# Performance work log

Measured on AMD Instinct MI355X. Metric: run time of the kernel, lower is better.

## Reference

```python
import jax, jax.numpy as jnp
import numpy as np

QUERY_DIM = 1024
KEY_DIM = 512
HIDDEN_DIM = 128
BATCH = 32
SEQ_LEN = 2048


def setup_inputs() -> dict:
    key = jax.random.key(0)
    k1, k2, k3, k4, k5 = jax.random.split(key, 5)
    query = jax.random.normal(k1, (BATCH, QUERY_DIM), dtype=jnp.float32)
    keys = jax.random.normal(k2, (BATCH, SEQ_LEN, KEY_DIM), dtype=jnp.float32)
    # nn.Linear weights, stored as (out, in) like torch; scaled ~ kaiming-uniform bound
    W1 = jax.random.normal(k3, (HIDDEN_DIM, QUERY_DIM), dtype=jnp.float32) / np.sqrt(QUERY_DIM)
    W2 = jax.random.normal(k4, (HIDDEN_DIM, KEY_DIM), dtype=jnp.float32) / np.sqrt(KEY_DIM)
    V = jax.random.normal(k5, (1, HIDDEN_DIM), dtype=jnp.float32) / np.sqrt(HIDDEN_DIM)
    return {"query": query, "keys": keys, "W1": W1, "W2": W2, "V": V}


def reference(query, keys, W1, W2, V):
    # query: [b, q], keys: [b, s, k]
    q_proj = jnp.einsum("bq,hq->bh", query, W1)          # [b, h]
    k_proj = jnp.einsum("bsk,hk->bsh", keys, W2)          # [b, s, h]
    hidden = jnp.tanh(q_proj[:, None, :] + k_proj)        # [b, s, h]
    score = jnp.einsum("bsh,oh->bs", hidden, V)           # [b, s] (o == 1)
    attention_weights = jax.nn.softmax(score, axis=1)     # [b, s]
    context = jnp.einsum("bs,bsk->bk", attention_weights, keys)  # [b, k]
    return (context, attention_weights)
```

## Files before the change

### kernel.cpp

```cpp
#include <hip/hip_runtime.h>

#define BATCH 32
#define SEQ   2048
#define KD    512
#define QD    1024
#define HD    128

#define BM 128
#define BK 32
#define NT (KD / BK)

typedef float    f32x4 __attribute__((ext_vector_type(4)));
typedef _Float16 f16x8 __attribute__((ext_vector_type(8)));
typedef unsigned int u32;

__device__ __forceinline__ u32 pack2h(float a, float b) {
    _Float16 ha = (_Float16)a, hb = (_Float16)b;
    unsigned short ua = __builtin_bit_cast(unsigned short, ha);
    unsigned short ub = __builtin_bit_cast(unsigned short, hb);
    return (u32)ua | ((u32)ub << 16);
}

__device__ __forceinline__ void cvt16(const f32x4 a[4], uint4& h0, uint4& h1) {
    h0 = make_uint4(pack2h(a[0][0], a[0][1]), pack2h(a[0][2], a[0][3]),
                    pack2h(a[1][0], a[1][1]), pack2h(a[1][2], a[1][3]));
    h1 = make_uint4(pack2h(a[2][0], a[2][1]), pack2h(a[2][2], a[2][3]),
                    pack2h(a[3][0], a[3][1]), pack2h(a[3][2], a[3][3]));
}

__device__ __forceinline__ void gload_lds16(const void* g, void* l) {
    __builtin_amdgcn_global_load_lds(
        (const __attribute__((address_space(1))) unsigned int*)g,
        (__attribute__((address_space(3))) unsigned int*)l, 16, 0, 0);
}

__global__ __launch_bounds__(256) void prep_kernel(
        const float* __restrict__ query, const float* __restrict__ W1,
        const float* __restrict__ W2, float* __restrict__ qp,
        char* __restrict__ w2img) {
    int blk = blockIdx.x;
    int tid = threadIdx.x;
    if (blk < 512) {
        int b = blk >> 4, hg = blk & 15;
        int wave = tid >> 6, lane = tid & 63;
        int h = hg * 8 + wave * 2 + (lane >> 5);
        int l32 = lane & 31;
        const float* q = query + (size_t)b * QD;
        const float* w = W1 + (size_t)h * QD;
        float acc = 0.f;
        #pragma unroll
        for (int i = 0; i < 8; ++i) {
            float4 qv = *(const float4*)(q + i * 128 + l32 * 4);
            float4 wv = *(const float4*)(w + i * 128 + l32 * 4);
            acc += qv.x * wv.x + qv.y * wv.y + qv.z * wv.z + qv.w * wv.w;
        }
        #pragma unroll
        for (int off = 16; off >= 1; off >>= 1) acc += __shfl_xor(acc, off);
        if (l32 == 0) qp[b * HD + h] = acc;
    } else {
        int c = blk - 512;
        int row = tid >> 1;
        int scol = (tid & 1) * 16;
        const float* src = W2 + (size_t)row * KD + c * BK + scol;
        f32x4 a[4];
        #pragma unroll
        for (int i = 0; i < 4; ++i) a[i] = *(const f32x4*)(src + i * 4);
        uint4 h0, h1;
        cvt16(a, h0, h1);
        int sw = (row & 7) << 4;
        int b0 = c * 8192 + ((row * 64 + scol * 2) ^ sw);
        int b1 = c * 8192 + ((row * 64 + scol * 2 + 16) ^ sw);
        *(uint4*)(w2img + b0) = h0;
        *(uint4*)(w2img + b1) = h1;
    }
}

__global__ __launch_bounds__(256, 2) void score_ctx_kernel(
        const float* __restrict__ keys, const char* __restrict__ w2img,
        const float* __restrict__ qp, const float* __restrict__ V,
        float* __restrict__ score_out, float* __restrict__ part_m,
        float* __restrict__ part_l, float* __restrict__ part_c) {
    __shared__ __align__(16) char lds[34048];
    char* A = lds;
    char* B = lds + 16384;
    float* sc  = (float*)(lds + 32768);
    float* pb  = (float*)(lds + 32768 + 512);
    float* red = (float*)(lds + 32768 + 1024);

    const int blk = blockIdx.x;
    const int m0  = blk * BM;
    const int b   = blk >> 4;
    const int tid = threadIdx.x;
    const int wave = tid >> 6;
    const int lane = tid & 63;
    const int l15  = lane & 15;
    const int l4   = lane >> 4;

    const int srow = tid >> 1;
    const int scol = (tid & 1) * 16;
    const int ssw  = (srow & 7) << 4;
    const int sb0  = (srow * 64 + scol * 2) ^ ssw;
    const int sb1  = (srow * 64 + scol * 2 + 16) ^ ssw;
    const float* asrc = keys + (size_t)(m0 + srow) * KD + scol;

    float qv[8], vv[8];
    #pragma unroll
    for (int hj = 0; hj < 8; ++hj) {
        qv[hj] = qp[b * HD + hj * 16 + l15];
        vv[hj] = V[hj * 16 + l15];
    }

    const int boff0 = (l15 * 64 + l4 * 16) ^ ((l15 & 7) << 4);
    const int aoff0 = boff0 + wave * 2048;
    const int aoff1 = aoff0 + 1024;

    f32x4 acc[2][8];
    #pragma unroll
    for (int mi = 0; mi < 2; ++mi)
        #pragma unroll
        for (int hj = 0; hj < 8; ++hj)
            acc[mi][hj] = (f32x4)0.f;

    {
        const char* g = w2img + wave * 2048 + lane * 16;
        gload_lds16(g,        B + wave * 2048);
        gload_lds16(g + 1024, B + wave * 2048 + 1024);
        f32x4 a[4];
        #pragma unroll
        for (int i = 0; i < 4; ++i) a[i] = *(const f32x4*)(asrc + i * 4);
        uint4 h0, h1;
        cvt16(a, h0, h1);
        *(uint4*)(A + sb0) = h0;
        *(uint4*)(A + sb1) = h1;
    }
    __syncthreads();

    for (int t = 0; t < NT; ++t) {
        const int cb = t & 1, nb = cb ^ 1;
        f32x4 a[4];
        if (t + 1 < NT) {
            const char* g = w2img + (t + 1) * 8192 + wave * 2048 + lane * 16;
            gload_lds16(g,        B + nb * 8192 + wave * 2048);
            gload_lds16(g + 1024, B + nb * 8192 + wave * 2048 + 1024);
            const float* s = asrc + (t + 1) * BK;
            #pragma unroll
            for (int i = 0; i < 4; ++i) a[i] = *(const f32x4*)(s + i * 4);
        }

        f16x8 ah0 = *(const f16x8*)(A + cb * 8192 + aoff0);
        f16x8 ah1 = *(const f16x8*)(A + cb * 8192 + aoff1);
        #pragma unroll
        for (int hj = 0; hj < 8; ++hj) {
            f16x8 bh = *(const f16x8*)(B + cb * 8192 + boff0 + hj * 1024);
            acc[0][hj] = __builtin_amdgcn_mfma_f32_16x16x32_f16(ah0, bh, acc[0][hj], 0, 0, 0);
            acc[1][hj] = __builtin_amdgcn_mfma_f32_16x16x32_f16(ah1, bh, acc[1][hj], 0, 0, 0);
        }

        if (t + 1 < NT) {
            uint4 h0, h1;
            cvt16(a, h0, h1);
            *(uint4*)(A + nb * 8192 + sb0) = h0;
            *(uint4*)(A + nb * 8192 + sb1) = h1;
        }
        __syncthreads();
    }

    #pragma unroll
    for (int mi = 0; mi < 2; ++mi) {
        #pragma unroll
        for (int j = 0; j < 4; ++j) {
            float p = 0.f;
            #pragma unroll
            for (int hj = 0; hj < 8; ++hj) {
                float x = qv[hj] + acc[mi][hj][j];
                float e = __expf(2.f * x);
                float th = 1.f - 2.f * __builtin_amdgcn_rcpf(1.f + e);
                p += th * vv[hj];
            }
            #pragma unroll
            for (int off = 1; off < 16; off <<= 1) p += __shfl_xor(p, off);
            if (l15 == 0) {
                int r = wave * 32 + mi * 16 + l4 * 4 + j;
                score_out[m0 + r] = p;
                sc[r] = p;
            }
        }
    }
    __syncthreads();

    float s_val = sc[tid & 127];
    float mx = s_val;
    #pragma unroll
    for (int off = 32; off >= 1; off >>= 1) mx = fmaxf(mx, __shfl_xor(mx, off));
    if (lane == 0) red[wave] = mx;
    __syncthreads();
    float m = fmaxf(fmaxf(red[0], red[1]), fmaxf(red[2], red[3]));
    float p = __expf(s_val - m);
    if (tid < 128) pb[tid] = p;
    float ps = p;
    #pragma unroll
    for (int off = 32; off >= 1; off >>= 1) ps += __shfl_xor(ps, off);
    if (lane == 0) red[4 + wave] = ps;
    __syncthreads();
    if (tid == 0) {
        part_m[blk] = m;
        part_l[blk] = red[4] + red[5];
    }

    int col = tid * 2;
    float c0 = 0.f, c1 = 0.f;
    const float* kb = keys + (size_t)m0 * KD + col;
    #pragma unroll 4
    for (int s = 0; s < BM; ++s) {
        float w = pb[s];
        float2 kv = *(const float2*)(kb + (size_t)s * KD);
        c0 = fmaf(w, kv.x, c0);
        c1 = fmaf(w, kv.y, c1);
    }
    *(float2*)(part_c + (size_t)blk * KD + col) = make_float2(c0, c1);
}

__global__ __launch_bounds__(256) void finalize_kernel(
        const float* __restrict__ part_m, const float* __restrict__ part_l,
        const float* __restrict__ part_c, float* __restrict__ ctx,
        float* __restrict__ wts) {
    int b = blockIdx.x;
    int tid = threadIdx.x;
    float M = -1e30f;
    #pragma unroll
    for (int i = 0; i < 16; ++i) M = fmaxf(M, part_m[b * 16 + i]);
    float e[16];
    float L = 0.f;
    #pragma unroll
    for (int i = 0; i < 16; ++i) {
        e[i] = __expf(part_m[b * 16 + i] - M);
        L += e[i] * part_l[b * 16 + i];
    }
    float invL = 1.f / L;
    #pragma unroll
    for (int r = 0; r < 8; ++r) {
        int s = tid + r * 256;
        float scv = wts[b * SEQ + s];
        wts[b * SEQ + s] = __expf(scv - M) * invL;
    }
    #pragma unroll
    for (int g = 0; g < 2; ++g) {
        int col = tid + g * 256;
        float acc = 0.f;
        #pragma unroll
        for (int i = 0; i < 16; ++i)
            acc += e[i] * part_c[(size_t)(b * 16 + i) * KD + col];
        ctx[b * KD + col] = acc * invL;
    }
}

extern "C" void kernel_launch(void* const* d_in, const int* in_sizes, int n_in,
                              void* d_out, int out_size, void* d_ws, size_t ws_size,
                              hipStream_t stream) {
    const float* query = (const float*)d_in[0];
    const float* keys  = (const float*)d_in[1];
    const float* W1    = (const float*)d_in[2];
    const float* W2    = (const float*)d_in[3];
    const float* V     = (const float*)d_in[4];

    float* ctx = (float*)d_out;
    float* wts = (float*)d_out + BATCH * KD;

    char* wsb   = (char*)d_ws;
    float* qp   = (float*)wsb;
    char* w2img = wsb + 16 * 1024;
    float* part_m = (float*)(wsb + 144 * 1024);
    float* part_l = (float*)(wsb + 146 * 1024);
    float* part_c = (float*)(wsb + 148 * 1024);

    prep_kernel<<<528, 256, 0, stream>>>(query, W1, W2, qp, w2img);
    score_ctx_kernel<<<(BATCH * SEQ) / BM, 256, 0, stream>>>(
        keys, w2img, qp, V, wts, part_m, part_l, part_c);
    finalize_kernel<<<BATCH, 256, 0, stream>>>(part_m, part_l, part_c, ctx, wts);
}
```

Before: 52.01 us.

## Replace LDS-staged GEMM with single-wave register-pipelined MFMA blocks over 32-row chunks

The score kernel now uses one 64-thread wave per 32-row chunk, launching 2048 blocks instead of 512. Keys and the pre-laid-out fp16 W2 fragments are loaded straight into registers with a 3-deep and 2-deep software prefetch, so LDS staging and per-step barriers disappear. The softmax reduction within a chunk is done with wave shuffles, and the context partial uses wider vector loads. In exchange each block re-reads all of W2 from global or cache, there are four times as many partial results for finalize to merge, and per-wave register pressure is higher.

```diff
diff --git a/kernel.cpp b/kernel.cpp
--- a/kernel.cpp
+++ b/kernel.cpp
@@ -6,9 +6,8 @@
 #define QD    1024
 #define HD    128
 
-#define BM 128
-#define BK 32
-#define NT (KD / BK)
+#define NT 16
+#define NCHUNK 64
 
 typedef float    f32x4 __attribute__((ext_vector_type(4)));
 typedef _Float16 f16x8 __attribute__((ext_vector_type(8)));
@@ -21,17 +20,10 @@
     return (u32)ua | ((u32)ub << 16);
 }
 
-__device__ __forceinline__ void cvt16(const f32x4 a[4], uint4& h0, uint4& h1) {
-    h0 = make_uint4(pack2h(a[0][0], a[0][1]), pack2h(a[0][2], a[0][3]),
-                    pack2h(a[1][0], a[1][1]), pack2h(a[1][2], a[1][3]));
-    h1 = make_uint4(pack2h(a[2][0], a[2][1]), pack2h(a[2][2], a[2][3]),
-                    pack2h(a[3][0], a[3][1]), pack2h(a[3][2], a[3][3]));
-}
-
-__device__ __forceinline__ void gload_lds16(const void* g, void* l) {
-    __builtin_amdgcn_global_load_lds(
-        (const __attribute__((address_space(1))) unsigned int*)g,
-        (__attribute__((address_space(3))) unsigned int*)l, 16, 0, 0);
+__device__ __forceinline__ f16x8 cvtA(const float4& r0, const float4& r1) {
+    uint4 u = make_uint4(pack2h(r0.x, r0.y), pack2h(r0.z, r0.w),
+                         pack2h(r1.x, r1.y), pack2h(r1.z, r1.w));
+    return __builtin_bit_cast(f16x8, u);
 }
 
 __global__ __launch_bounds__(256) void prep_kernel(
@@ -58,50 +50,81 @@
         for (int off = 16; off >= 1; off >>= 1) acc += __shfl_xor(acc, off);
         if (l32 == 0) qp[b * HD + h] = acc;
     } else {
-        int c = blk - 512;
-        int row = tid >> 1;
-        int scol = (tid & 1) * 16;
-        const float* src = W2 + (size_t)row * KD + c * BK + scol;
-        f32x4 a[4];
-        #pragma unroll
-        for (int i = 0; i < 4; ++i) a[i] = *(const f32x4*)(src + i * 4);
-        uint4 h0, h1;
-        cvt16(a, h0, h1);
-        int sw = (row & 7) << 4;
-        int b0 = c * 8192 + ((row * 64 + scol * 2) ^ sw);
-        int b1 = c * 8192 + ((row * 64 + scol * 2 + 16) ^ sw);
-        *(uint4*)(w2img + b0) = h0;
-        *(uint4*)(w2img + b1) = h1;
-    }
-}
-
-__global__ __launch_bounds__(256, 2) void score_ctx_kernel(
+        int t = blk - 512;
+        #pragma unroll
+        for (int rep = 0; rep < 2; ++rep) {
+            int f  = tid + rep * 256;
+            int hj = f >> 6;
+            int ln = f & 63;
+            int r  = hj * 16 + (ln & 15);
+            int c  = t * 32 + (ln >> 4) * 8;
+            const float* src = W2 + (size_t)r * KD + c;
+            float4 v0 = *(const float4*)(src);
+            float4 v1 = *(const float4*)(src + 4);
+            uint4 u = make_uint4(pack2h(v0.x, v0.y), pack2h(v0.z, v0.w),
+                                 pack2h(v1.x, v1.y), pack2h(v1.z, v1.w));
+            *(uint4*)(w2img + ((size_t)t * 512 + f) * 16) = u;
+        }
+    }
+}
+
+__global__ __launch_bounds__(64, 2) void score_ctx_kernel(
         const float* __restrict__ keys, const char* __restrict__ w2img,
         const float* __restrict__ qp, const float* __restrict__ V,
         float* __restrict__ score_out, float* __restrict__ part_m,
         float* __restrict__ part_l, float* __restrict__ part_c) {
-    __shared__ __align__(16) char lds[34048];
-    char* A = lds;
-    char* B = lds + 16384;
-    float* sc  = (float*)(lds + 32768);
-    float* pb  = (float*)(lds + 32768 + 512);
-    float* red = (float*)(lds + 32768 + 1024);
-
-    const int blk = blockIdx.x;
-    const int m0  = blk * BM;
-    const int b   = blk >> 4;
-    const int tid = threadIdx.x;
-    const int wave = tid >> 6;
-    const int lane = tid & 63;
+    __shared__ float pb[32];
+
+    const int blk  = blockIdx.x;
+    const int m0   = blk * 32;
+    const int b    = blk >> 6;
+    const int lane = threadIdx.x;
     const int l15  = lane & 15;
     const int l4   = lane >> 4;
 
-    const int srow = tid >> 1;
-    const int scol = (tid & 1) * 16;
-    const int ssw  = (srow & 7) << 4;
-    const int sb0  = (srow * 64 + scol * 2) ^ ssw;
-    const int sb1  = (srow * 64 + scol * 2 + 16) ^ ssw;
-    const float* asrc = keys + (size_t)(m0 + srow) * KD + scol;
+    const float* arow0 = keys + (size_t)(m0 + l15) * KD + l4 * 8;
+    const float* arow1 = arow0 + 16 * KD;
+    const char*  bbase = w2img + lane * 16;
+
+    f32x4 acc[2][8];
+    #pragma unroll
+    for (int mi = 0; mi < 2; ++mi)
+        #pragma unroll
+        for (int hj = 0; hj < 8; ++hj)
+            acc[mi][hj] = (f32x4)0.f;
+
+    float4 ka[3][4];
+    f16x8  kb[2][8];
+
+#define KA(slot, t) { \
+        ka[slot][0] = *(const float4*)(arow0 + (t) * 32); \
+        ka[slot][1] = *(const float4*)(arow0 + (t) * 32 + 4); \
+        ka[slot][2] = *(const float4*)(arow1 + (t) * 32); \
+        ka[slot][3] = *(const float4*)(arow1 + (t) * 32 + 4); }
+#define KB(slot, t) { \
+        _Pragma("unroll") \
+        for (int hj = 0; hj < 8; ++hj) \
+            kb[slot][hj] = *(const f16x8*)(bbase + (t) * 8192 + hj * 1024); }
+
+    KA(0, 0)
+    KA(1, 1)
+    KB(0, 0)
+
+    #pragma unroll
+    for (int t = 0; t < NT; ++t) {
+        if (t + 2 < NT) KA((t + 2) % 3, t + 2)
+        if (t + 1 < NT) KB((t + 1) & 1, t + 1)
+
+        f16x8 af0 = cvtA(ka[t % 3][0], ka[t % 3][1]);
+        f16x8 af1 = cvtA(ka[t % 3][2], ka[t % 3][3]);
+        #pragma unroll
+        for (int hj = 0; hj < 8; ++hj) {
+            acc[0][hj] = __builtin_amdgcn_mfma_f32_16x16x32_f16(af0, kb[t & 1][hj], acc[0][hj], 0, 0, 0);
+            acc[1][hj] = __builtin_amdgcn_mfma_f32_16x16x32_f16(af1, kb[t & 1][hj], acc[1][hj], 0, 0, 0);
+        }
+    }
+#undef KA
+#undef KB
 
     float qv[8], vv[8];
     #pragma unroll
@@ -110,61 +133,7 @@
         vv[hj] = V[hj * 16 + l15];
     }
 
-    const int boff0 = (l15 * 64 + l4 * 16) ^ ((l15 & 7) << 4);
-    const int aoff0 = boff0 + wave * 2048;
-    const int aoff1 = aoff0 + 1024;
-
-    f32x4 acc[2][8];
-    #pragma unroll
-    for (int mi = 0; mi < 2; ++mi)
-        #pragma unroll
-        for (int hj = 0; hj < 8; ++hj)
-            acc[mi][hj] = (f32x4)0.f;
-
-    {
-        const char* g = w2img + wave * 2048 + lane * 16;
-        gload_lds16(g,        B + wave * 2048);
-        gload_lds16(g + 1024, B + wave * 2048 + 1024);
-        f32x4 a[4];
-        #pragma unroll
-        for (int i = 0; i < 4; ++i) a[i] = *(const f32x4*)(asrc + i * 4);
-        uint4 h0, h1;
-        cvt16(a, h0, h1);
-        *(uint4*)(A + sb0) = h0;
-        *(uint4*)(A + sb1) = h1;
-    }
-    __syncthreads();
-
-    for (int t = 0; t < NT; ++t) {
-        const int cb = t & 1, nb = cb ^ 1;
-        f32x4 a[4];
-        if (t + 1 < NT) {
-            const char* g = w2img + (t + 1) * 8192 + wave * 2048 + lane * 16;
-            gload_lds16(g,        B + nb * 8192 + wave * 2048);
-            gload_lds16(g + 1024, B + nb * 8192 + wave * 2048 + 1024);
-            const float* s = asrc + (t + 1) * BK;
-            #pragma unroll
-            for (int i = 0; i < 4; ++i) a[i] = *(const f32x4*)(s + i * 4);
-        }
-
-        f16x8 ah0 = *(const f16x8*)(A + cb * 8192 + aoff0);
-        f16x8 ah1 = *(const f16x8*)(A + cb * 8192 + aoff1);
-        #pragma unroll
-        for (int hj = 0; hj < 8; ++hj) {
-            f16x8 bh = *(const f16x8*)(B + cb * 8192 + boff0 + hj * 1024);
-            acc[0][hj] = __builtin_amdgcn_mfma_f32_16x16x32_f16(ah0, bh, acc[0][hj], 0, 0, 0);
-            acc[1][hj] = __builtin_amdgcn_mfma_f32_16x16x32_f16(ah1, bh, acc[1][hj], 0, 0, 0);
-        }
-
-        if (t + 1 < NT) {
-            uint4 h0, h1;
-            cvt16(a, h0, h1);
-            *(uint4*)(A + nb * 8192 + sb0) = h0;
-            *(uint4*)(A + nb * 8192 + sb1) = h1;
-        }
-        __syncthreads();
-    }
-
+    float p8[8];
     #pragma unroll
     for (int mi = 0; mi < 2; ++mi) {
         #pragma unroll
@@ -179,63 +148,67 @@
             }
             #pragma unroll
             for (int off = 1; off < 16; off <<= 1) p += __shfl_xor(p, off);
-            if (l15 == 0) {
-                int r = wave * 32 + mi * 16 + l4 * 4 + j;
-                score_out[m0 + r] = p;
-                sc[r] = p;
-            }
-        }
+            p8[mi * 4 + j] = p;
+            if (l15 == 0) score_out[m0 + mi * 16 + l4 * 4 + j] = p;
+        }
+    }
+
+    float mx = p8[0];
+    #pragma unroll
+    for (int i = 1; i < 8; ++i) mx = fmaxf(mx, p8[i]);
+    mx = fmaxf(mx, __shfl_xor(mx, 16));
+    mx = fmaxf(mx, __shfl_xor(mx, 32));
+    float e8[8], ls = 0.f;
+    #pragma unroll
+    for (int i = 0; i < 8; ++i) {
+        e8[i] = __expf(p8[i] - mx);
+        ls += e8[i];
+    }
+    ls += __shfl_xor(ls, 16);
+    ls += __shfl_xor(ls, 32);
+    if (lane == 0) {
+        part_m[blk] = mx;
+        part_l[blk] = ls;
+    }
+    if (l15 == 0) {
+        #pragma unroll
+        for (int mi = 0; mi < 2; ++mi)
+            #pragma unroll
+            for (int j = 0; j < 4; ++j)
+                pb[mi * 16 + l4 * 4 + j] = e8[mi * 4 + j];
     }
     __syncthreads();
 
-    float s_val = sc[tid & 127];
-    float mx = s_val;
-    #pragma unroll
-    for (int off = 32; off >= 1; off >>= 1) mx = fmaxf(mx, __shfl_xor(mx, off));
-    if (lane == 0) red[wave] = mx;
-    __syncthreads();
-    float m = fmaxf(fmaxf(red[0], red[1]), fmaxf(red[2], red[3]));
-    float p = __expf(s_val - m);
-    if (tid < 128) pb[tid] = p;
-    float ps = p;
-    #pragma unroll
-    for (int off = 32; off >= 1; off >>= 1) ps += __shfl_xor(ps, off);
-    if (lane == 0) red[4 + wave] = ps;
-    __syncthreads();
-    if (tid == 0) {
-        part_m[blk] = m;
-        part_l[blk] = red[4] + red[5];
-    }
-
-    int col = tid * 2;
-    float c0 = 0.f, c1 = 0.f;
-    const float* kb = keys + (size_t)m0 * KD + col;
-    #pragma unroll 4
-    for (int s = 0; s < BM; ++s) {
+    int c0 = lane * 8;
+    f32x4 a0 = (f32x4)0.f, a1 = (f32x4)0.f;
+    const float* kb2 = keys + (size_t)m0 * KD + c0;
+    #pragma unroll 8
+    for (int s = 0; s < 32; ++s) {
         float w = pb[s];
-        float2 kv = *(const float2*)(kb + (size_t)s * KD);
-        c0 = fmaf(w, kv.x, c0);
-        c1 = fmaf(w, kv.y, c1);
-    }
-    *(float2*)(part_c + (size_t)blk * KD + col) = make_float2(c0, c1);
+        f32x4 k0 = *(const f32x4*)(kb2 + (size_t)s * KD);
+        f32x4 k1 = *(const f32x4*)(kb2 + (size_t)s * KD + 4);
+        a0 += w * k0;
+        a1 += w * k1;
+    }
+    *(f32x4*)(part_c + (size_t)blk * KD + c0) = a0;
+    *(f32x4*)(part_c + (size_t)blk * KD + c0 + 4) = a1;
 }
 
 __global__ __launch_bounds__(256) void finalize_kernel(
         const float* __restrict__ part_m, const float* __restrict__ part_l,
         const float* __restrict__ part_c, float* __restrict__ ctx,
         float* __restrict__ wts) {
+    __shared__ float eS[NCHUNK];
     int b = blockIdx.x;
     int tid = threadIdx.x;
     float M = -1e30f;
-    #pragma unroll
-    for (int i = 0; i < 16; ++i) M = fmaxf(M, part_m[b * 16 + i]);
-    float e[16];
+    #pragma unroll 8
+    for (int i = 0; i < NCHUNK; ++i) M = fmaxf(M, part_m[b * NCHUNK + i]);
+    if (tid < NCHUNK) eS[tid] = __expf(part_m[b * NCHUNK + tid] - M);
+    __syncthreads();
     float L = 0.f;
-    #pragma unroll
-    for (int i = 0; i < 16; ++i) {
-        e[i] = __expf(part_m[b * 16 + i] - M);
-        L += e[i] * part_l[b * 16 + i];
-    }
+    #pragma unroll 8
+    for (int i = 0; i < NCHUNK; ++i) L += eS[i] * part_l[b * NCHUNK + i];
     float invL = 1.f / L;
     #pragma unroll
     for (int r = 0; r < 8; ++r) {
@@ -243,15 +216,17 @@
         float scv = wts[b * SEQ + s];
         wts[b * SEQ + s] = __expf(scv - M) * invL;
     }
-    #pragma unroll
-    for (int g = 0; g < 2; ++g) {
-        int col = tid + g * 256;
-        float acc = 0.f;
-        #pragma unroll
-        for (int i = 0; i < 16; ++i)
-            acc += e[i] * part_c[(size_t)(b * 16 + i) * KD + col];
-        ctx[b * KD + col] = acc * invL;
-    }
+    int col = tid * 2;
+    float c0 = 0.f, c1 = 0.f;
+    #pragma unroll 8
+    for (int i = 0; i < NCHUNK; ++i) {
+        float w = eS[i];
+        float2 pc = *(const float2*)(part_c + (size_t)(b * NCHUNK + i) * KD + col);
+        c0 = fmaf(w, pc.x, c0);
+        c1 = fmaf(w, pc.y, c1);
+    }
+    ctx[b * KD + col]     = c0 * invL;
+    ctx[b * KD + col + 1] = c1 * invL;
 }
 
 extern "C" void kernel_launch(void* const* d_in, const int* in_sizes, int n_in,
@@ -266,15 +241,15 @@
     float* ctx = (float*)d_out;
     float* wts = (float*)d_out + BATCH * KD;
 
-    char* wsb   = (char*)d_ws;
-    float* qp   = (float*)wsb;
-    char* w2img = wsb + 16 * 1024;
+    char* wsb     = (char*)d_ws;
+    float* qp     = (float*)wsb;
+    char*  w2img  = wsb + 16 * 1024;
     float* part_m = (float*)(wsb + 144 * 1024);
-    float* part_l = (float*)(wsb + 146 * 1024);
-    float* part_c = (float*)(wsb + 148 * 1024);
+    float* part_l = (float*)(wsb + 152 * 1024);
+    float* part_c = (float*)(wsb + 160 * 1024);
 
     prep_kernel<<<528, 256, 0, stream>>>(query, W1, W2, qp, w2img);
-    score_ctx_kernel<<<(BATCH * SEQ) / BM, 256, 0, stream>>>(
+    score_ctx_kernel<<<BATCH * NCHUNK, 64, 0, stream>>>(
         keys, w2img, qp, V, wts, part_m, part_l, part_c);
     finalize_kernel<<<BATCH, 256, 0, stream>>>(part_m, part_l, part_c, ctx, wts);
 }
```

New measurement: 75.45 us. 45.1% more time.

## Stream fp32 keys directly to LDS with triple-buffered async loads

Applied to the files above, without the earlier changes.

The main GEMM loop now loads fp32 key tiles straight into LDS with global_load_lds alongside the W2 image, using a three-slot ring buffer with explicit vmcnt waits and a single barrier per step. The fp16 conversion moves to the consumer side after the LDS read, and MFMA sections are wrapped in raised wave priority. The goal is to overlap global loads with compute more deeply and remove register staging and the convert-and-store step from the critical path. In exchange LDS use rises to about 73 KB, which may limit occupancy to 2 blocks per CU, and the hand-written waitcnt/barrier protocol is fragile.

```diff
diff --git a/kernel.cpp b/kernel.cpp
--- a/kernel.cpp
+++ b/kernel.cpp
@@ -6,9 +6,9 @@
 #define QD    1024
 #define HD    128
 
-#define BM 128
-#define BK 32
-#define NT (KD / BK)
+#define NT 16
+#define ROWS 128
+#define NCHUNK 16
 
 typedef float    f32x4 __attribute__((ext_vector_type(4)));
 typedef _Float16 f16x8 __attribute__((ext_vector_type(8)));
@@ -26,6 +26,12 @@
                     pack2h(a[1][0], a[1][1]), pack2h(a[1][2], a[1][3]));
     h1 = make_uint4(pack2h(a[2][0], a[2][1]), pack2h(a[2][2], a[2][3]),
                     pack2h(a[3][0], a[3][1]), pack2h(a[3][2], a[3][3]));
+}
+
+__device__ __forceinline__ f16x8 cvtA4(const f32x4& r0, const f32x4& r1) {
+    uint4 u = make_uint4(pack2h(r0[0], r0[1]), pack2h(r0[2], r0[3]),
+                         pack2h(r1[0], r1[1]), pack2h(r1[2], r1[3]));
+    return __builtin_bit_cast(f16x8, u);
 }
 
 __device__ __forceinline__ void gload_lds16(const void* g, void* l) {
@@ -61,7 +67,7 @@
         int c = blk - 512;
         int row = tid >> 1;
         int scol = (tid & 1) * 16;
-        const float* src = W2 + (size_t)row * KD + c * BK + scol;
+        const float* src = W2 + (size_t)row * KD + c * 32 + scol;
         f32x4 a[4];
         #pragma unroll
         for (int i = 0; i < 4; ++i) a[i] = *(const f32x4*)(src + i * 4);
@@ -80,89 +86,80 @@
         const float* __restrict__ qp, const float* __restrict__ V,
         float* __restrict__ score_out, float* __restrict__ part_m,
         float* __restrict__ part_l, float* __restrict__ part_c) {
-    __shared__ __align__(16) char lds[34048];
-    char* A = lds;
-    char* B = lds + 16384;
-    float* sc  = (float*)(lds + 32768);
-    float* pb  = (float*)(lds + 32768 + 512);
-    float* red = (float*)(lds + 32768 + 1024);
-
-    const int blk = blockIdx.x;
-    const int m0  = blk * BM;
-    const int b   = blk >> 4;
-    const int tid = threadIdx.x;
+    __shared__ __align__(16) char slab[3][24576];
+    __shared__ float sc[ROWS];
+    __shared__ float pb[ROWS];
+    __shared__ float red[8];
+
+    const int blk  = blockIdx.x;
+    const int m0   = blk * ROWS;
+    const int b    = blk >> 4;
+    const int tid  = threadIdx.x;
     const int wave = tid >> 6;
     const int lane = tid & 63;
     const int l15  = lane & 15;
     const int l4   = lane >> 4;
 
-    const int srow = tid >> 1;
-    const int scol = (tid & 1) * 16;
-    const int ssw  = (srow & 7) << 4;
-    const int sb0  = (srow * 64 + scol * 2) ^ ssw;
-    const int sb1  = (srow * 64 + scol * 2 + 16) ^ ssw;
-    const float* asrc = keys + (size_t)(m0 + srow) * KD + scol;
+    const char* asrc0 = (const char*)keys
+        + (size_t)(m0 + wave * 32 + (lane >> 3)) * (KD * 4)
+        + (((lane & 7) * 16) ^ ((lane >> 3) << 4));
+
+    const int swz = (l15 & 7) << 4;
+    const int ar0 = (wave * 32 + l15) * 128;
+    const int ac0 = (l4 * 32) ^ swz;
+    const int ac1 = (l4 * 32 + 16) ^ swz;
+    const int boff0 = 16384 + ((l15 * 64 + l4 * 16) ^ swz);
+
+    f32x4 acc[2][8];
+    #pragma unroll
+    for (int mi = 0; mi < 2; ++mi)
+        #pragma unroll
+        for (int hj = 0; hj < 8; ++hj)
+            acc[mi][hj] = (f32x4)0.f;
+
+#define STAGE(slot, t) { \
+        char* as_ = slab[slot]; \
+        gload_lds16(asrc0 + 0 * 16384 + (t) * 128, as_ + wave * 4096 + 0 * 1024); \
+        gload_lds16(asrc0 + 1 * 16384 + (t) * 128, as_ + wave * 4096 + 1 * 1024); \
+        gload_lds16(asrc0 + 2 * 16384 + (t) * 128, as_ + wave * 4096 + 2 * 1024); \
+        gload_lds16(asrc0 + 3 * 16384 + (t) * 128, as_ + wave * 4096 + 3 * 1024); \
+        const char* g_ = w2img + (t) * 8192 + wave * 2048 + lane * 16; \
+        gload_lds16(g_,        as_ + 16384 + wave * 2048); \
+        gload_lds16(g_ + 1024, as_ + 16384 + wave * 2048 + 1024); }
+
+    STAGE(0, 0)
+
+    #pragma unroll
+    for (int t = 0; t < NT; ++t) {
+        const int cs = t % 3;
+        if (t + 1 < NT) STAGE((t + 1) % 3, t + 1)
+
+        if (t + 1 < NT) asm volatile("s_waitcnt vmcnt(6)" ::: "memory");
+        else            asm volatile("s_waitcnt vmcnt(0)" ::: "memory");
+        asm volatile("s_barrier" ::: "memory");
+
+        const char* as = slab[cs];
+        #pragma unroll
+        for (int mi = 0; mi < 2; ++mi) {
+            f32x4 lo = *(const f32x4*)(as + ar0 + mi * 2048 + ac0);
+            f32x4 hi = *(const f32x4*)(as + ar0 + mi * 2048 + ac1);
+            f16x8 af = cvtA4(lo, hi);
+            __builtin_amdgcn_s_setprio(1);
+            #pragma unroll
+            for (int hj = 0; hj < 8; ++hj) {
+                f16x8 bh = *(const f16x8*)(as + boff0 + hj * 1024);
+                acc[mi][hj] = __builtin_amdgcn_mfma_f32_16x16x32_f16(af, bh, acc[mi][hj], 0, 0, 0);
+            }
+            __builtin_amdgcn_s_setprio(0);
+        }
+    }
+#undef STAGE
 
     float qv[8], vv[8];
     #pragma unroll
     for (int hj = 0; hj < 8; ++hj) {
         qv[hj] = qp[b * HD + hj * 16 + l15];
         vv[hj] = V[hj * 16 + l15];
-    }
-
-    const int boff0 = (l15 * 64 + l4 * 16) ^ ((l15 & 7) << 4);
-    const int aoff0 = boff0 + wave * 2048;
-    const int aoff1 = aoff0 + 1024;
-
-    f32x4 acc[2][8];
-    #pragma unroll
-    for (int mi = 0; mi < 2; ++mi)
-        #pragma unroll
-        for (int hj = 0; hj < 8; ++hj)
-            acc[mi][hj] = (f32x4)0.f;
-
-    {
-        const char* g = w2img + wave * 2048 + lane * 16;
-        gload_lds16(g,        B + wave * 2048);
-        gload_lds16(g + 1024, B + wave * 2048 + 1024);
-        f32x4 a[4];
-        #pragma unroll
-        for (int i = 0; i < 4; ++i) a[i] = *(const f32x4*)(asrc + i * 4);
-        uint4 h0, h1;
-        cvt16(a, h0, h1);
-        *(uint4*)(A + sb0) = h0;
-        *(uint4*)(A + sb1) = h1;
-    }
-    __syncthreads();
-
-    for (int t = 0; t < NT; ++t) {
-        const int cb = t & 1, nb = cb ^ 1;
-        f32x4 a[4];
-        if (t + 1 < NT) {
-            const char* g = w2img + (t + 1) * 8192 + wave * 2048 + lane * 16;
-            gload_lds16(g,        B + nb * 8192 + wave * 2048);
-            gload_lds16(g + 1024, B + nb * 8192 + wave * 2048 + 1024);
-            const float* s = asrc + (t + 1) * BK;
-            #pragma unroll
-            for (int i = 0; i < 4; ++i) a[i] = *(const f32x4*)(s + i * 4);
-        }
-
-        f16x8 ah0 = *(const f16x8*)(A + cb * 8192 + aoff0);
-        f16x8 ah1 = *(const f16x8*)(A + cb * 8192 + aoff1);
-        #pragma unroll
-        for (int hj = 0; hj < 8; ++hj) {
-            f16x8 bh = *(const f16x8*)(B + cb * 8192 + boff0 + hj * 1024);
-            acc[0][hj] = __builtin_amdgcn_mfma_f32_16x16x32_f16(ah0, bh, acc[0][hj], 0, 0, 0);
-            acc[1][hj] = __builtin_amdgcn_mfma_f32_16x16x32_f16(ah1, bh, acc[1][hj], 0, 0, 0);
-        }
-
-        if (t + 1 < NT) {
-            uint4 h0, h1;
-            cvt16(a, h0, h1);
-            *(uint4*)(A + nb * 8192 + sb0) = h0;
-            *(uint4*)(A + nb * 8192 + sb1) = h1;
-        }
-        __syncthreads();
     }
 
     #pragma unroll
@@ -209,11 +206,11 @@
 
     int col = tid * 2;
     float c0 = 0.f, c1 = 0.f;
-    const float* kb = keys + (size_t)m0 * KD + col;
+    const float* kb2 = keys + (size_t)m0 * KD + col;
     #pragma unroll 4
-    for (int s = 0; s < BM; ++s) {
+    for (int s = 0; s < ROWS; ++s) {
         float w = pb[s];
-        float2 kv = *(const float2*)(kb + (size_t)s * KD);
+        float2 kv = *(const float2*)(kb2 + (size_t)s * KD);
         c0 = fmaf(w, kv.x, c0);
         c1 = fmaf(w, kv.y, c1);
     }
@@ -228,13 +225,13 @@
     int tid = threadIdx.x;
     float M = -1e30f;
     #pragma unroll
-    for (int i = 0; i < 16; ++i) M = fmaxf(M, part_m[b * 16 + i]);
-    float e[16];
+    for (int i = 0; i < NCHUNK; ++i) M = fmaxf(M, part_m[b * NCHUNK + i]);
+    float e[NCHUNK];
     float L = 0.f;
     #pragma unroll
-    for (int i = 0; i < 16; ++i) {
-        e[i] = __expf(part_m[b * 16 + i] - M);
-        L += e[i] * part_l[b * 16 + i];
+    for (int i = 0; i < NCHUNK; ++i) {
+        e[i] = __expf(part_m[b * NCHUNK + i] - M);
+        L += e[i] * part_l[b * NCHUNK + i];
     }
     float invL = 1.f / L;
     #pragma unroll
@@ -248,8 +245,8 @@
         int col = tid + g * 256;
         float acc = 0.f;
         #pragma unroll
-        for (int i = 0; i < 16; ++i)
-            acc += e[i] * part_c[(size_t)(b * 16 + i) * KD + col];
+        for (int i = 0; i < NCHUNK; ++i)
+            acc += e[i] * part_c[(size_t)(b * NCHUNK + i) * KD + col];
         ctx[b * KD + col] = acc * invL;
     }
 }
@@ -266,15 +263,15 @@
     float* ctx = (float*)d_out;
     float* wts = (float*)d_out + BATCH * KD;
 
-    char* wsb   = (char*)d_ws;
-    float* qp   = (float*)wsb;
-    char* w2img = wsb + 16 * 1024;
+    char* wsb     = (char*)d_ws;
+    float* qp     = (float*)wsb;
+    char*  w2img  = wsb + 16 * 1024;
     float* part_m = (float*)(wsb + 144 * 1024);
     float* part_l = (float*)(wsb + 146 * 1024);
     float* part_c = (float*)(wsb + 148 * 1024);
 
     prep_kernel<<<528, 256, 0, stream>>>(query, W1, W2, qp, w2img);
-    score_ctx_kernel<<<(BATCH * SEQ) / BM, 256, 0, stream>>>(
+    score_ctx_kernel<<<BATCH * NCHUNK, 256, 0, stream>>>(
         keys, w2img, qp, V, wts, part_m, part_l, part_c);
     finalize_kernel<<<BATCH, 256, 0, stream>>>(part_m, part_l, part_c, ctx, wts);
 }
```

After: 52.49 us. About the same (+0.9%).
